# Kernel optimization log

Measured on AMD Instinct MI355X. Metric: run time of the kernel, lower is better.

Reference implementation:

```python
import jax, jax.numpy as jnp
import numpy as np

D_MODEL = 1024
N_HEADS = 16
D_HEAD = D_MODEL // N_HEADS


def setup_inputs() -> dict:
    key = jax.random.key(0)
    ks = jax.random.split(key, 9)
    s = 1.0 / np.sqrt(D_MODEL)
    def lin(kw, kb):
        W = jax.random.uniform(kw, (D_MODEL, D_MODEL), jnp.float32, -s, s)
        b = jax.random.uniform(kb, (D_MODEL,), jnp.float32, -s, s)
        return W, b
    Wq, bq = lin(ks[0], ks[1])
    Wk, bk = lin(ks[2], ks[3])
    Wv, bv = lin(ks[4], ks[5])
    Wo, bo = lin(ks[6], ks[7])
    x = jax.random.normal(ks[8], (4, 2048, D_MODEL), jnp.float32)
    return {"x": x, "Wq": Wq, "bq": bq, "Wk": Wk, "bk": bk,
            "Wv": Wv, "bv": bv, "Wo": Wo, "bo": bo}


def reference(x, Wq, bq, Wk, bk, Wv, bv, Wo, bo):
    B, T, C = x.shape
    # torch Linear: y = x @ W.T + b
    Q = x @ Wq.T + bq
    K = x @ Wk.T + bk
    V = x @ Wv.T + bv
    # [B, H, T, Dh]
    Q = Q.reshape(B, T, N_HEADS, D_HEAD).transpose(0, 2, 1, 3)
    K = K.reshape(B, T, N_HEADS, D_HEAD).transpose(0, 2, 1, 3)
    V = V.reshape(B, T, N_HEADS, D_HEAD).transpose(0, 2, 1, 3)
    scale = jnp.float32(np.sqrt(D_HEAD))
    scores = jnp.einsum('bhqd,bhkd->bhqk', Q, K) / scale
    causal = jnp.tril(jnp.ones((T, T), dtype=bool))  # True where allowed
    scores = jnp.where(causal, scores, jnp.float32(-jnp.inf))
    attn = jax.nn.softmax(scores, axis=-1)
    out = jnp.einsum('bhqk,bhkd->bhqd', attn, V)
    out = out.transpose(0, 2, 1, 3).reshape(B, T, C)
    return out @ Wo.T + bo
```

## Files before the change

### kernel.cpp

```cpp
#include <hip/hip_runtime.h>
#include <hip/hip_bf16.h>


typedef float f32x4 __attribute__((ext_vector_type(4)));
typedef __bf16 bf16x8 __attribute__((ext_vector_type(8)));

#define DEVI __device__ __forceinline__

#define QSCALE 0.1803368801111204f

template<int N> struct IC { static constexpr int value = N; };

DEVI ushort f2b(float x) {
  __hip_bfloat16 h = __float2bfloat16(x);
  return __builtin_bit_cast(ushort, h);
}

DEVI unsigned int pkbf(float a, float b) {
#if __has_builtin(__builtin_amdgcn_cvt_pk_bf16_f32)
  typedef __bf16 bf16x2 __attribute__((ext_vector_type(2)));
  bf16x2 r = __builtin_amdgcn_cvt_pk_bf16_f32(a, b);
  return __builtin_bit_cast(unsigned int, r);
#else
  return (unsigned int)f2b(a) | ((unsigned int)f2b(b) << 16);
#endif
}

DEVI bf16x8 ldsFrag(const ushort* p) {
  return __builtin_bit_cast(bf16x8, *(const uint4*)p);
}

DEVI f32x4 mfma16(bf16x8 a, bf16x8 b, f32x4 c) {
  return __builtin_amdgcn_mfma_f32_16x16x32_bf16(a, b, c, 0, 0, 0);
}

DEVI void gload_lds16(const ushort* g, ushort* l) {
  __builtin_amdgcn_global_load_lds(
      (const __attribute__((address_space(1))) unsigned int*)g,
      (__attribute__((address_space(3))) unsigned int*)l, 16, 0, 0);
}

#define SBAR() do { __builtin_amdgcn_sched_barrier(0); \
                    __builtin_amdgcn_s_barrier();      \
                    __builtin_amdgcn_sched_barrier(0); } while (0)

__global__ void k_cvtAll(const float4* __restrict__ x,
                         const float4* __restrict__ w0, const float4* __restrict__ w1,
                         const float4* __restrict__ w2, const float4* __restrict__ w3,
                         ushort4* __restrict__ xb, ushort4* __restrict__ wcat) {
  const int blk = blockIdx.x;
  const int i = blk * 256 + threadIdx.x;
  float4 f;
  ushort4* dst;
  int di;
  if (blk < 8192) {
    f = x[i]; dst = xb; di = i;
  } else {
    const int wi = i - 8192 * 256;
    const int sel = wi >> 18;
    const float4* src = (sel == 0) ? w0 : (sel == 1) ? w1 : (sel == 2) ? w2 : w3;
    f = src[wi & 262143]; dst = wcat; di = wi;
  }
  ushort4 o;
  o.x = f2b(f.x); o.y = f2b(f.y); o.z = f2b(f.z); o.w = f2b(f.w);
  dst[di] = o;
}

__global__ __launch_bounds__(512, 2)
void k_gemm256(const ushort* __restrict__ A, const ushort* __restrict__ W,
               const float* __restrict__ b0, const float* __restrict__ b1,
               const float* __restrict__ b2,
               ushort* __restrict__ oQ, ushort* __restrict__ oK,
               ushort* __restrict__ oV) {
  __shared__ ushort As[2][256 * 64];
  __shared__ ushort Bs[2][256 * 64];
  const int tid = threadIdx.x;
  const int wave = tid >> 6, lane = tid & 63;
  const int col = lane & 15, quad = lane >> 4;
  const int id = blockIdx.x;
  const int L = (id & 7) * 48 + (id >> 3);
  const int m0 = (L & 31) * 256;
  const int n0 = (L >> 5) * 256;
  const int wm = (wave >> 2) * 128, wn = (wave & 3) * 64;
  const int matId = n0 >> 10;

  const int grow = lane >> 3;
  const int gchunk = ((lane & 7) ^ grow) * 8;
  const int cswz = col & 7;
  const ushort* Ag = A + (size_t)(m0 + wave * 32 + grow) * 1024 + gchunk;
  const ushort* Wg = W + (size_t)(n0 + wave * 32 + grow) * 1024 + gchunk;

  f32x4 acc[8][4] = {};
  bf16x8 bfr[4];

  auto stageHalf = [&](int t1, int hf) {
    const int buf = t1 & 1;
    const int ks = t1 * 64;
#pragma unroll
    for (int u = 2 * hf; u < 2 * hf + 2; ++u) {
      gload_lds16(Ag + (size_t)u * 8 * 1024 + ks, &As[buf][(wave * 32 + u * 8) * 64]);
      gload_lds16(Wg + (size_t)u * 8 * 1024 + ks, &Bs[buf][(wave * 32 + u * 8) * 64]);
    }
  };

  auto kloop = [&](auto swc) {
    constexpr bool SW = (decltype(swc)::value != 0);
    auto phase = [&](int p, int h, int kk, bool rdB, auto stg) {
      const int ko = ((kk * 4 + quad) ^ cswz) * 8;
      bf16x8 af[4];
#pragma unroll
      for (int i = 0; i < 4; ++i)
        af[i] = ldsFrag(&As[p][(wm + h * 64 + i * 16 + col) * 64 + ko]);
      if (rdB) {
#pragma unroll
        for (int j = 0; j < 4; ++j)
          bfr[j] = ldsFrag(&Bs[p][(wn + j * 16 + col) * 64 + ko]);
      }
      stg();
      SBAR();
      asm volatile("s_waitcnt lgkmcnt(0)" ::: "memory");
      __builtin_amdgcn_sched_barrier(0);
      __builtin_amdgcn_s_setprio(1);
#pragma unroll
      for (int i = 0; i < 4; ++i)
#pragma unroll
        for (int j = 0; j < 4; ++j) {
          if constexpr (SW)
            acc[h * 4 + i][j] = mfma16(bfr[j], af[i], acc[h * 4 + i][j]);
          else
            acc[h * 4 + i][j] = mfma16(af[i], bfr[j], acc[h * 4 + i][j]);
        }
      __builtin_amdgcn_s_setprio(0);
      SBAR();
    };

    stageHalf(0, 0); stageHalf(0, 1);
    asm volatile("s_waitcnt vmcnt(0)" ::: "memory");
    SBAR();

    for (int t = 0; t < 16; ++t) {
      const int p = t & 1;
      const bool st = (t < 15);
      phase(p, 0, 0, true,  [&] { if (st) stageHalf(t + 1, 0); });
      phase(p, 1, 0, false, [&] { if (st) stageHalf(t + 1, 1); });
      phase(p, 0, 1, true,  [&] {});
      {
        const int ko = ((1 * 4 + quad) ^ cswz) * 8;
        bf16x8 af[4];
#pragma unroll
        for (int i = 0; i < 4; ++i)
          af[i] = ldsFrag(&As[p][(wm + 64 + i * 16 + col) * 64 + ko]);
        SBAR();
        asm volatile("s_waitcnt lgkmcnt(0)" ::: "memory");
        __builtin_amdgcn_sched_barrier(0);
        __builtin_amdgcn_s_setprio(1);
#pragma unroll
        for (int i = 0; i < 4; ++i)
#pragma unroll
          for (int j = 0; j < 4; ++j) {
            if constexpr (SW)
              acc[4 + i][j] = mfma16(bfr[j], af[i], acc[4 + i][j]);
            else
              acc[4 + i][j] = mfma16(af[i], bfr[j], acc[4 + i][j]);
          }
        __builtin_amdgcn_s_setprio(0);
        if (st) { asm volatile("s_waitcnt vmcnt(0)" ::: "memory"); }
        SBAR();
      }
    }
  };

  if (matId < 2) kloop(IC<1>{}); else kloop(IC<0>{});

  if (matId < 2) {
    ushort* dst = (matId == 0) ? oQ : oK;
    const float* bias = (matId == 0) ? b0 : b1;
    const float sc = (matId == 0) ? QSCALE : 1.0f;
#pragma unroll
    for (int h = 0; h < 2; ++h)
#pragma unroll
      for (int j = 0; j < 4; ++j) {
        const int nl = (n0 & 1023) + wn + j * 16 + quad * 4;
        const int hh = nl >> 6, dh0 = nl & 63;
        const float4 bb = *(const float4*)&bias[nl];
#pragma unroll
        for (int i = 0; i < 4; ++i) {
          const int m = m0 + wm + h * 64 + i * 16 + col;
          const int b = m >> 11, t = m & 2047;
          ushort4 pk;
          pk.x = f2b((acc[h * 4 + i][j][0] + bb.x) * sc);
          pk.y = f2b((acc[h * 4 + i][j][1] + bb.y) * sc);
          pk.z = f2b((acc[h * 4 + i][j][2] + bb.z) * sc);
          pk.w = f2b((acc[h * 4 + i][j][3] + bb.w) * sc);
          *(ushort4*)&dst[(((size_t)(b * 16 + hh) * 2048) + t) * 64 + dh0] = pk;
        }
      }
  } else {
#pragma unroll
    for (int h = 0; h < 2; ++h)
#pragma unroll
      for (int j = 0; j < 4; ++j) {
        const int nl = (n0 & 1023) + wn + j * 16 + col;
        const int hh = nl >> 6, dh = nl & 63;
        const float bn = b2[nl];
#pragma unroll
        for (int i = 0; i < 4; ++i) {
          const int mBase = m0 + wm + h * 64 + i * 16 + quad * 4;
          const int b = mBase >> 11, t = mBase & 2047;
          ushort4 pk;
          pk.x = f2b(acc[h * 4 + i][j][0] + bn);
          pk.y = f2b(acc[h * 4 + i][j][1] + bn);
          pk.z = f2b(acc[h * 4 + i][j][2] + bn);
          pk.w = f2b(acc[h * 4 + i][j][3] + bn);
          *(ushort4*)&oV[(((size_t)(b * 16 + hh) * 64) + dh) * 2048 + t] = pk;
        }
      }
  }
}

__global__ __launch_bounds__(512, 2)
void k_gemmP(const ushort* __restrict__ A, const ushort* __restrict__ W,
             const float* __restrict__ b0, float* __restrict__ outF) {
  __shared__ ushort As[3 * 128 * 64];
  __shared__ ushort Bs[3 * 256 * 64];
  const int tid = threadIdx.x;
  const int wave = tid >> 6, lane = tid & 63;
  const int col = lane & 15, quad = lane >> 4;
  const int id = blockIdx.x;
  const int s_ = id >> 3;
  const int m0 = ((id & 7) * 8 + (s_ & 7)) * 128;
  const int n0 = (s_ >> 3) * 256;
  const int wm = (wave >> 2) * 64, wn = (wave & 3) * 64;
  f32x4 acc[4][4] = {};

  const int grow = lane >> 3;
  const int gchunk = ((lane & 7) ^ grow) * 8;
  const int cswz = col & 7;
  const ushort* Ag = A + (size_t)(m0 + wave * 16 + grow) * 1024 + gchunk;
  const ushort* Wg = W + (size_t)(n0 + wave * 32 + grow) * 1024 + gchunk;
  ushort* AsW = &As[wave * 1024];
  ushort* BsW = &Bs[wave * 2048];

  auto stageA = [&](int ks, int sb) {
    gload_lds16(Ag + ks,        AsW + sb * 8192);
    gload_lds16(Ag + ks + 8192, AsW + sb * 8192 + 512);
  };
  auto stageBh = [&](int ks, int sb, int h) {
    const ushort* sp = Wg + ks + h * 16384;
    ushort* dp = BsW + sb * 16384 + h * 1024;
    gload_lds16(sp,        dp);
    gload_lds16(sp + 8192, dp + 512);
  };

  auto phase = [&](int cur, int kk, auto stagef) {
    const int ko = ((kk * 4 + quad) ^ cswz) * 8;
    const ushort* Ab = &As[cur * 8192];
    const ushort* Bb = &Bs[cur * 16384];
    bf16x8 af[4], bfr[4];
#pragma unroll
    for (int i = 0; i < 4; ++i)
      af[i] = ldsFrag(&Ab[(wm + i * 16 + col) * 64 + ko]);
#pragma unroll
    for (int j = 0; j < 4; ++j)
      bfr[j] = ldsFrag(&Bb[(wn + j * 16 + col) * 64 + ko]);
    stagef();
    SBAR();
    __builtin_amdgcn_s_setprio(1);
#pragma unroll
    for (int i = 0; i < 4; ++i)
#pragma unroll
      for (int j = 0; j < 4; ++j)
        acc[i][j] = mfma16(bfr[j], af[i], acc[i][j]);
    __builtin_amdgcn_s_setprio(0);
  };

  stageA(0, 0);  stageBh(0, 0, 0);  stageBh(0, 0, 1);
  stageA(64, 1); stageBh(64, 1, 0); stageBh(64, 1, 1);
  asm volatile("s_waitcnt vmcnt(6)" ::: "memory");
  SBAR();

  int r0 = 0, r1 = 1, r2 = 2;
  for (int t = 0; t < 14; ++t) {
    const int ks = (t + 2) * 64;
    phase(r0, 0, [&] { stageA(ks, r2); stageBh(ks, r2, 0); });
    SBAR();
    phase(r0, 1, [&] { stageBh(ks, r2, 1); });
    asm volatile("s_waitcnt vmcnt(6)" ::: "memory");
    SBAR();
    const int tmp = r0; r0 = r1; r1 = r2; r2 = tmp;
  }
  phase(r0, 0, [&] {});
  SBAR();
  phase(r0, 1, [&] {});
  asm volatile("s_waitcnt vmcnt(0)" ::: "memory");
  SBAR();
  phase(r1, 0, [&] {});
  SBAR();
  phase(r1, 1, [&] {});

#pragma unroll
  for (int j = 0; j < 4; ++j) {
    const int nb = n0 + wn + j * 16 + quad * 4;
    const float4 bb = *(const float4*)&b0[nb];
#pragma unroll
    for (int i = 0; i < 4; ++i) {
      const int m = m0 + wm + i * 16 + col;
      float4 v;
      v.x = acc[i][j][0] + bb.x;
      v.y = acc[i][j][1] + bb.y;
      v.z = acc[i][j][2] + bb.z;
      v.w = acc[i][j][3] + bb.w;
      *(float4*)&outF[(size_t)m * 1024 + nb] = v;
    }
  }
}

__global__ __launch_bounds__(512, 4)
void k_attn(const ushort* __restrict__ Q, const ushort* __restrict__ K,
            const ushort* __restrict__ Vt, ushort* __restrict__ AO) {
  __shared__ ushort Ks[2 * 4096];
  __shared__ ushort Vs[2 * 4096];
  __shared__ ushort Os[512];
  __shared__ ushort Ps[16 * 16 * 72];
  const int tid = threadIdx.x;
  const int wave = tid >> 6, lane = tid & 63;
  const int col = lane & 15, quad = lane >> 4;
  const int id = blockIdx.x;
  const int bh = (id & 7) * 8 + ((id >> 3) & 7);
  const int g = id >> 6;
  const int t = (id < 256) ? (7 - g) : (g - 4);
  const int q0 = t * 256;
  const ushort* Qg = Q + (size_t)bh * 2048 * 64;
  const ushort* Kg = K + (size_t)bh * 2048 * 64;
  const ushort* Vg = Vt + (size_t)bh * 64 * 2048;

  if (tid < 128) {
    const ushort one = 0x3F80;
    ushort4 zv;
    if (tid < 8) { zv.x = one; zv.y = one; zv.z = one; zv.w = one; }
    else         { zv.x = 0;   zv.y = 0;   zv.z = 0;   zv.w = 0;   }
    *(ushort4*)&Os[tid * 4] = zv;
  }

  const int grow = lane >> 3;
  const int gchunk = ((lane & 7) ^ grow) * 8;
  const int cswz = col & 7;
  ushort* Pw0 = &Ps[((wave * 2 + 0) * 16 + col) * 72];
  ushort* Pw1 = &Ps[((wave * 2 + 1) * 16 + col) * 72];

  bf16x8 qf[2][2];
#pragma unroll
  for (int s = 0; s < 2; ++s) {
    const ushort* p = Qg + (q0 + wave * 32 + s * 16 + col) * 64 + quad * 8;
    qf[s][0] = __builtin_bit_cast(bf16x8, *(const uint4*)p);
    qf[s][1] = __builtin_bit_cast(bf16x8, *(const uint4*)(p + 32));
  }

  f32x4 o[2][4] = {};
  f32x4 la[2] = {};

  const ushort* kPtr = Kg + (wave * 8 + grow) * 64 + gchunk;
  const ushort* vPtr = Vg + (size_t)(wave * 8 + grow) * 2048 + gchunk;

  auto stage = [&](auto bufc) {
    constexpr int BUF = decltype(bufc)::value;
    gload_lds16(kPtr, &Ks[BUF * 4096 + wave * 512]);
    gload_lds16(vPtr, &Vs[BUF * 4096 + wave * 512]);
    kPtr += 64 * 64;
    vPtr += 64;
  };

  auto step = [&](auto bufc, auto maskc, int j0) {
    constexpr int BUF = decltype(bufc)::value;
    constexpr bool MASKED = (decltype(maskc)::value != 0);
    const ushort* Kb = &Ks[BUF * 4096];
    const ushort* Vb = &Vs[BUF * 4096];
    bf16x8 kf[4][2];
#pragma unroll
    for (int i = 0; i < 4; ++i) {
      kf[i][0] = ldsFrag(&Kb[(i * 16 + col) * 64 + (((0 * 4 + quad) ^ cswz) * 8)]);
      kf[i][1] = ldsFrag(&Kb[(i * 16 + col) * 64 + (((1 * 4 + quad) ^ cswz) * 8)]);
    }
#pragma unroll
    for (int s = 0; s < 2; ++s) {
      ushort* Pw = s ? Pw1 : Pw0;
      const int dlim = MASKED ? (q0 + wave * 32 + s * 16 + col - j0 - quad * 4) : 0;
#pragma unroll
      for (int i = 0; i < 4; ++i) {
        f32x4 z = {0.f, 0.f, 0.f, 0.f};
        f32x4 sv = mfma16(kf[i][0], qf[s][0], z);
        sv = mfma16(kf[i][1], qf[s][1], sv);
        if (MASKED) {
#pragma unroll
          for (int r = 0; r < 4; ++r)
            if (i * 16 + r > dlim) sv[r] = -1e30f;
        }
        f32x4 pv;
#pragma unroll
        for (int r = 0; r < 4; ++r) pv[r] = __builtin_amdgcn_exp2f(sv[r]);
        uint2 pk;
        pk.x = pkbf(pv[0], pv[1]);
        pk.y = pkbf(pv[2], pv[3]);
        *(uint2*)&Pw[i * 16 + quad * 4] = pk;
      }
    }
    bf16x8 osf = ldsFrag(&Os[col * 32 + quad * 8]);
#pragma unroll
    for (int c = 0; c < 2; ++c) {
      bf16x8 pb0 = ldsFrag(&Pw0[c * 32 + quad * 8]);
      bf16x8 pb1 = ldsFrag(&Pw1[c * 32 + quad * 8]);
      la[0] = mfma16(osf, pb0, la[0]);
      la[1] = mfma16(osf, pb1, la[1]);
#pragma unroll
      for (int i = 0; i < 4; ++i) {
        bf16x8 vf = ldsFrag(&Vb[(i * 16 + col) * 64 + (((c * 4 + quad) ^ cswz) * 8)]);
        o[0][i] = mfma16(vf, pb0, o[0][i]);
        o[1][i] = mfma16(vf, pb1, o[1][i]);
      }
    }
  };

  __syncthreads();
  stage(IC<0>{});
  for (int it2 = 0; it2 < 2 * t; ++it2) {
    __syncthreads();
    stage(IC<1>{});
    step(IC<0>{}, IC<0>{}, 0);
    __syncthreads();
    stage(IC<0>{});
    step(IC<1>{}, IC<0>{}, 0);
  }
  __syncthreads();
  stage(IC<1>{});
  step(IC<0>{}, IC<1>{}, q0);
  __syncthreads();
  stage(IC<0>{});
  if (wave >= 2) step(IC<1>{}, IC<1>{}, q0 + 64);
  __syncthreads();
  stage(IC<1>{});
  if (wave >= 4) step(IC<0>{}, IC<1>{}, q0 + 128);
  __syncthreads();
  if (wave >= 6) step(IC<1>{}, IC<1>{}, q0 + 192);

  const float invs[2] = {1.0f / __shfl(la[0][0], col), 1.0f / __shfl(la[1][0], col)};
  const int b = bh >> 4, h = bh & 15;
#pragma unroll
  for (int s = 0; s < 2; ++s) {
    const float inv = invs[s];
    const int tq = q0 + wave * 32 + s * 16 + col;
    ushort* dst = AO + (size_t)(b * 2048 + tq) * 1024 + h * 64;
#pragma unroll
    for (int i = 0; i < 4; ++i) {
      f32x4 v = o[s][i];
      ushort4 pk;
      pk.x = f2b(v[0] * inv);
      pk.y = f2b(v[1] * inv);
      pk.z = f2b(v[2] * inv);
      pk.w = f2b(v[3] * inv);
      *(ushort4*)&dst[i * 16 + quad * 4] = pk;
    }
  }
}

extern "C" void kernel_launch(void* const* d_in, const int* in_sizes, int n_in,
                              void* d_out, int out_size, void* d_ws, size_t ws_size,
                              hipStream_t stream) {
  const float* x  = (const float*)d_in[0];
  const float* Wq = (const float*)d_in[1];
  const float* bq = (const float*)d_in[2];
  const float* Wk = (const float*)d_in[3];
  const float* bk = (const float*)d_in[4];
  const float* Wv = (const float*)d_in[5];
  const float* bv = (const float*)d_in[6];
  const float* Wo = (const float*)d_in[7];
  const float* bo = (const float*)d_in[8];
  float* out = (float*)d_out;

  char* ws = (char*)d_ws;
  ushort* xb    = (ushort*)ws;
  ushort* Wcat  = (ushort*)(ws + (size_t)16 * 1024 * 1024);
  ushort* Wob   = Wcat + (size_t)3 * 1024 * 1024;
  ushort* Qh    = (ushort*)(ws + (size_t)24 * 1024 * 1024);
  ushort* Kh    = Qh + (size_t)8192 * 1024;
  ushort* Vt    = Kh + (size_t)8192 * 1024;
  ushort* AO    = Vt + (size_t)8192 * 1024;

  k_cvtAll<<<12288, 256, 0, stream>>>((const float4*)x,
                                      (const float4*)Wq, (const float4*)Wk,
                                      (const float4*)Wv, (const float4*)Wo,
                                      (ushort4*)xb, (ushort4*)Wcat);

  k_gemm256<<<384, 512, 0, stream>>>(xb, Wcat, bq, bk, bv, Qh, Kh, Vt);

  k_attn<<<512, 512, 0, stream>>>(Qh, Kh, Vt, AO);

  k_gemmP<<<256, 512, 0, stream>>>(AO, Wob, bo, out);
}
```

Before: 254.8 us.

## Retile QKV GEMM to 256x384 tiles mixing Q/K and V columns per block

Each block of the QKV projection now computes a 256-row by 384-column tile: 256 columns from Q or K plus 128 columns from V. This cuts the grid from 384 to 256 blocks, i.e. one wave of blocks at 2 blocks per CU on 256 CUs, and removes the separate V-specialized path. The intent is to avoid a partial second wave and to reuse each A tile across more output columns. In exchange the kernel needs 80 KB of LDS for B and more accumulator registers, which may hurt occupancy or cause spills.

```diff
diff --git a/kernel.cpp b/kernel.cpp
--- a/kernel.cpp
+++ b/kernel.cpp
@@ -67,120 +67,115 @@
 }
 
 __global__ __launch_bounds__(512, 2)
-void k_gemm256(const ushort* __restrict__ A, const ushort* __restrict__ W,
-               const float* __restrict__ b0, const float* __restrict__ b1,
-               const float* __restrict__ b2,
+void k_gemmQKV(const ushort* __restrict__ A, const ushort* __restrict__ W,
+               const float* __restrict__ bq, const float* __restrict__ bk,
+               const float* __restrict__ bv,
                ushort* __restrict__ oQ, ushort* __restrict__ oK,
                ushort* __restrict__ oV) {
   __shared__ ushort As[2][256 * 64];
-  __shared__ ushort Bs[2][256 * 64];
+  __shared__ ushort Bs[2][384 * 64];
   const int tid = threadIdx.x;
   const int wave = tid >> 6, lane = tid & 63;
   const int col = lane & 15, quad = lane >> 4;
   const int id = blockIdx.x;
-  const int L = (id & 7) * 48 + (id >> 3);
-  const int m0 = (L & 31) * 256;
-  const int n0 = (L >> 5) * 256;
-  const int wm = (wave >> 2) * 128, wn = (wave & 3) * 64;
-  const int matId = n0 >> 10;
+  const int xcd = id & 7, idx = id >> 3;
+  const int m0 = (xcd * 4 + (idx & 3)) * 256;
+  const int nb = idx >> 2;
+  const int wm = (wave >> 2) * 128;
+  const int wn = (wave & 3) * 64;
+  const int wnv = (wave & 3) * 32;
+  const bool matQ = (nb < 4);
 
   const int grow = lane >> 3;
   const int gchunk = ((lane & 7) ^ grow) * 8;
   const int cswz = col & 7;
   const ushort* Ag = A + (size_t)(m0 + wave * 32 + grow) * 1024 + gchunk;
-  const ushort* Wg = W + (size_t)(n0 + wave * 32 + grow) * 1024 + gchunk;
-
-  f32x4 acc[8][4] = {};
-  bf16x8 bfr[4];
-
-  auto stageHalf = [&](int t1, int hf) {
+
+  auto bptr = [&](int u) {
+    const int br = wave * 48 + u * 8;
+    const int wr = (br < 256) ? (nb * 256 + br + grow)
+                              : (2048 + nb * 128 + (br - 256) + grow);
+    return W + (size_t)wr * 1024 + gchunk;
+  };
+
+  f32x4 aq[8][4] = {};
+  f32x4 av[8][2] = {};
+  bf16x8 bfr[4], bfv[2];
+
+  auto stage6 = [&](int t1) {
     const int buf = t1 & 1;
     const int ks = t1 * 64;
 #pragma unroll
-    for (int u = 2 * hf; u < 2 * hf + 2; ++u) {
+    for (int u = 0; u < 4; ++u)
       gload_lds16(Ag + (size_t)u * 8 * 1024 + ks, &As[buf][(wave * 32 + u * 8) * 64]);
-      gload_lds16(Wg + (size_t)u * 8 * 1024 + ks, &Bs[buf][(wave * 32 + u * 8) * 64]);
-    }
-  };
-
-  auto kloop = [&](auto swc) {
-    constexpr bool SW = (decltype(swc)::value != 0);
-    auto phase = [&](int p, int h, int kk, bool rdB, auto stg) {
-      const int ko = ((kk * 4 + quad) ^ cswz) * 8;
-      bf16x8 af[4];
-#pragma unroll
-      for (int i = 0; i < 4; ++i)
-        af[i] = ldsFrag(&As[p][(wm + h * 64 + i * 16 + col) * 64 + ko]);
-      if (rdB) {
-#pragma unroll
-        for (int j = 0; j < 4; ++j)
-          bfr[j] = ldsFrag(&Bs[p][(wn + j * 16 + col) * 64 + ko]);
-      }
-      stg();
-      SBAR();
-      asm volatile("s_waitcnt lgkmcnt(0)" ::: "memory");
-      __builtin_amdgcn_sched_barrier(0);
-      __builtin_amdgcn_s_setprio(1);
-#pragma unroll
-      for (int i = 0; i < 4; ++i)
-#pragma unroll
-        for (int j = 0; j < 4; ++j) {
-          if constexpr (SW)
-            acc[h * 4 + i][j] = mfma16(bfr[j], af[i], acc[h * 4 + i][j]);
-          else
-            acc[h * 4 + i][j] = mfma16(af[i], bfr[j], acc[h * 4 + i][j]);
-        }
-      __builtin_amdgcn_s_setprio(0);
-      SBAR();
-    };
-
-    stageHalf(0, 0); stageHalf(0, 1);
-    asm volatile("s_waitcnt vmcnt(0)" ::: "memory");
+#pragma unroll
+    for (int u = 0; u < 2; ++u)
+      gload_lds16(bptr(u) + ks, &Bs[buf][(wave * 48 + u * 8) * 64]);
+  };
+  auto stage4 = [&](int t1) {
+    const int buf = t1 & 1;
+    const int ks = t1 * 64;
+#pragma unroll
+    for (int u = 2; u < 6; ++u)
+      gload_lds16(bptr(u) + ks, &Bs[buf][(wave * 48 + u * 8) * 64]);
+  };
+
+  auto phase = [&](int p, int h, int kk, bool rdB, int dr, auto stg) {
+    const int ko = ((kk * 4 + quad) ^ cswz) * 8;
+    bf16x8 af[4];
+#pragma unroll
+    for (int i = 0; i < 4; ++i)
+      af[i] = ldsFrag(&As[p][(wm + h * 64 + i * 16 + col) * 64 + ko]);
+    if (rdB) {
+#pragma unroll
+      for (int j = 0; j < 4; ++j)
+        bfr[j] = ldsFrag(&Bs[p][(wn + j * 16 + col) * 64 + ko]);
+#pragma unroll
+      for (int j = 0; j < 2; ++j)
+        bfv[j] = ldsFrag(&Bs[p][(256 + wnv + j * 16 + col) * 64 + ko]);
+    }
+    stg();
     SBAR();
-
-    for (int t = 0; t < 16; ++t) {
-      const int p = t & 1;
-      const bool st = (t < 15);
-      phase(p, 0, 0, true,  [&] { if (st) stageHalf(t + 1, 0); });
-      phase(p, 1, 0, false, [&] { if (st) stageHalf(t + 1, 1); });
-      phase(p, 0, 1, true,  [&] {});
-      {
-        const int ko = ((1 * 4 + quad) ^ cswz) * 8;
-        bf16x8 af[4];
-#pragma unroll
-        for (int i = 0; i < 4; ++i)
-          af[i] = ldsFrag(&As[p][(wm + 64 + i * 16 + col) * 64 + ko]);
-        SBAR();
-        asm volatile("s_waitcnt lgkmcnt(0)" ::: "memory");
-        __builtin_amdgcn_sched_barrier(0);
-        __builtin_amdgcn_s_setprio(1);
-#pragma unroll
-        for (int i = 0; i < 4; ++i)
-#pragma unroll
-          for (int j = 0; j < 4; ++j) {
-            if constexpr (SW)
-              acc[4 + i][j] = mfma16(bfr[j], af[i], acc[4 + i][j]);
-            else
-              acc[4 + i][j] = mfma16(af[i], bfr[j], acc[4 + i][j]);
-          }
-        __builtin_amdgcn_s_setprio(0);
-        if (st) { asm volatile("s_waitcnt vmcnt(0)" ::: "memory"); }
-        SBAR();
-      }
-    }
-  };
-
-  if (matId < 2) kloop(IC<1>{}); else kloop(IC<0>{});
-
-  if (matId < 2) {
-    ushort* dst = (matId == 0) ? oQ : oK;
-    const float* bias = (matId == 0) ? b0 : b1;
-    const float sc = (matId == 0) ? QSCALE : 1.0f;
+    asm volatile("s_waitcnt lgkmcnt(0)" ::: "memory");
+    __builtin_amdgcn_sched_barrier(0);
+    __builtin_amdgcn_s_setprio(1);
+#pragma unroll
+    for (int i = 0; i < 4; ++i)
+#pragma unroll
+      for (int j = 0; j < 4; ++j)
+        aq[h * 4 + i][j] = mfma16(bfr[j], af[i], aq[h * 4 + i][j]);
+#pragma unroll
+    for (int i = 0; i < 4; ++i)
+#pragma unroll
+      for (int j = 0; j < 2; ++j)
+        av[h * 4 + i][j] = mfma16(af[i], bfv[j], av[h * 4 + i][j]);
+    __builtin_amdgcn_s_setprio(0);
+    if (dr) { asm volatile("s_waitcnt vmcnt(0)" ::: "memory"); }
+    SBAR();
+  };
+
+  stage6(0); stage4(0);
+  asm volatile("s_waitcnt vmcnt(0)" ::: "memory");
+  SBAR();
+
+  for (int t = 0; t < 16; ++t) {
+    const int p = t & 1;
+    const bool st = (t < 15);
+    phase(p, 0, 0, true,  0,  [&] { if (st) stage6(t + 1); });
+    phase(p, 1, 0, false, 0,  [&] { if (st) stage4(t + 1); });
+    phase(p, 0, 1, true,  0,  [&] {});
+    phase(p, 1, 1, false, st ? 1 : 0, [&] {});
+  }
+
+  {
+    ushort* dst = matQ ? oQ : oK;
+    const float* bias = matQ ? bq : bk;
+    const float sc = matQ ? QSCALE : 1.0f;
 #pragma unroll
     for (int h = 0; h < 2; ++h)
 #pragma unroll
       for (int j = 0; j < 4; ++j) {
-        const int nl = (n0 & 1023) + wn + j * 16 + quad * 4;
+        const int nl = (nb & 3) * 256 + wn + j * 16 + quad * 4;
         const int hh = nl >> 6, dh0 = nl & 63;
         const float4 bb = *(const float4*)&bias[nl];
 #pragma unroll
@@ -188,30 +183,31 @@
           const int m = m0 + wm + h * 64 + i * 16 + col;
           const int b = m >> 11, t = m & 2047;
           ushort4 pk;
-          pk.x = f2b((acc[h * 4 + i][j][0] + bb.x) * sc);
-          pk.y = f2b((acc[h * 4 + i][j][1] + bb.y) * sc);
-          pk.z = f2b((acc[h * 4 + i][j][2] + bb.z) * sc);
-          pk.w = f2b((acc[h * 4 + i][j][3] + bb.w) * sc);
+          pk.x = f2b((aq[h * 4 + i][j][0] + bb.x) * sc);
+          pk.y = f2b((aq[h * 4 + i][j][1] + bb.y) * sc);
+          pk.z = f2b((aq[h * 4 + i][j][2] + bb.z) * sc);
+          pk.w = f2b((aq[h * 4 + i][j][3] + bb.w) * sc);
           *(ushort4*)&dst[(((size_t)(b * 16 + hh) * 2048) + t) * 64 + dh0] = pk;
         }
       }
-  } else {
+  }
+  {
 #pragma unroll
     for (int h = 0; h < 2; ++h)
 #pragma unroll
-      for (int j = 0; j < 4; ++j) {
-        const int nl = (n0 & 1023) + wn + j * 16 + col;
+      for (int j = 0; j < 2; ++j) {
+        const int nl = nb * 128 + wnv + j * 16 + col;
         const int hh = nl >> 6, dh = nl & 63;
-        const float bn = b2[nl];
+        const float bn = bv[nl];
 #pragma unroll
         for (int i = 0; i < 4; ++i) {
           const int mBase = m0 + wm + h * 64 + i * 16 + quad * 4;
           const int b = mBase >> 11, t = mBase & 2047;
           ushort4 pk;
-          pk.x = f2b(acc[h * 4 + i][j][0] + bn);
-          pk.y = f2b(acc[h * 4 + i][j][1] + bn);
-          pk.z = f2b(acc[h * 4 + i][j][2] + bn);
-          pk.w = f2b(acc[h * 4 + i][j][3] + bn);
+          pk.x = f2b(av[h * 4 + i][j][0] + bn);
+          pk.y = f2b(av[h * 4 + i][j][1] + bn);
+          pk.z = f2b(av[h * 4 + i][j][2] + bn);
+          pk.w = f2b(av[h * 4 + i][j][3] + bn);
           *(ushort4*)&oV[(((size_t)(b * 16 + hh) * 64) + dh) * 2048 + t] = pk;
         }
       }
@@ -490,7 +486,7 @@
                                       (const float4*)Wv, (const float4*)Wo,
                                       (ushort4*)xb, (ushort4*)Wcat);
 
-  k_gemm256<<<384, 512, 0, stream>>>(xb, Wcat, bq, bk, bv, Qh, Kh, Vt);
+  k_gemmQKV<<<256, 512, 0, stream>>>(xb, Wcat, bq, bk, bv, Qh, Kh, Vt);
 
   k_attn<<<512, 512, 0, stream>>>(Qh, Kh, Vt, AO);
 
```

New measurement: 245.9 us. 1.04x faster.
